# Optimization experiments

Measured on AMD Instinct MI355X. Metric: run time of the kernel, lower is better.

Reference implementation:

```python
import jax, jax.numpy as jnp
import numpy as np

N_NODES = 100000
N_EDGES = 1600000
F_IN = 5
F_HID = 64
F_OUT = 72
NEG_SLOPE = 0.2  # PyG GATConv default


def setup_inputs() -> dict:
    key = jax.random.key(0)
    ks = jax.random.split(key, 8)
    x = jax.random.normal(ks[0], (N_NODES, F_IN), dtype=jnp.float32)
    edge_index = jax.random.randint(ks[1], (2, N_EDGES), 0, N_NODES, dtype=jnp.int64)
    # GATConv params (heads=1, concat=True)
    W = jax.random.normal(ks[2], (F_IN, F_HID), dtype=jnp.float32) * (1.0 / np.sqrt(F_IN))
    att_src = jax.random.normal(ks[3], (F_HID,), dtype=jnp.float32) * (1.0 / np.sqrt(F_HID))
    att_dst = jax.random.normal(ks[4], (F_HID,), dtype=jnp.float32) * (1.0 / np.sqrt(F_HID))
    b_gat = jnp.zeros((F_HID,), dtype=jnp.float32)
    # feature_extractor: Linear(64 -> 72) + ReLU
    W_fc = jax.random.normal(ks[5], (F_HID, F_OUT), dtype=jnp.float32) * (1.0 / np.sqrt(F_HID))
    b_fc = jnp.zeros((F_OUT,), dtype=jnp.float32)
    return {"x": x, "edge_index": edge_index, "W": W, "att_src": att_src,
            "att_dst": att_dst, "b_gat": b_gat, "W_fc": W_fc, "b_fc": b_fc}


def _gat_forward(x, edge_index, W, att_src, att_dst, b_gat, W_fc, b_fc):
    N = x.shape[0]
    h = x @ W  # [N, F_HID]
    # add self loops (PyG GATConv default add_self_loops=True)
    loops = jnp.arange(N, dtype=edge_index.dtype)
    src = jnp.concatenate([edge_index[0], loops])  # [E + N]
    dst = jnp.concatenate([edge_index[1], loops])
    # per-node attention halves, gathered per edge
    a_s = h @ att_src  # [N]
    a_d = h @ att_dst  # [N]
    e = a_s[src] + a_d[dst]  # [E + N]
    e = jnp.where(e > 0, e, NEG_SLOPE * e)  # LeakyReLU
    # edge-softmax grouped by destination node
    m = jax.ops.segment_max(e, dst, num_segments=N)  # self loops => no empty segment
    ex = jnp.exp(e - m[dst])
    denom = jax.ops.segment_sum(ex, dst, num_segments=N)
    alpha = ex / (denom[dst] + 1e-16)
    # weighted scatter-add aggregation
    out = jax.ops.segment_sum(alpha[:, None] * h[src], dst, num_segments=N) + b_gat  # [N, F_HID]
    pooled = jnp.mean(out, axis=0, keepdims=True)  # [1, F_HID]
    return jax.nn.relu(pooled @ W_fc + b_fc)  # [1, F_OUT]


def reference(x, edge_index, W, att_src, att_dst, b_gat, W_fc, b_fc):
    return _gat_forward(x, edge_index, W, att_src, att_dst, b_gat, W_fc, b_fc)
```

## Files before the change

kernel.cpp:

```cpp
#include <hip/hip_runtime.h>


#define NR 25
#define RSHIFT 12
#define RSZ 4096
#define RMASK 4095
#define BBIN 256
#define BINTHR 1024
#define T 8
#define PXE_BLOCKS 512

__global__ __launch_bounds__(256) void k_att(
    const float* __restrict__ x, const float* __restrict__ W,
    const float* __restrict__ att_src, const float* __restrict__ att_dst,
    float* __restrict__ a_s, float* __restrict__ a_d, int N) {
  const int lane = threadIdx.x & 63;
  const int n = blockIdx.x * 4 + (threadIdx.x >> 6);
  if (n >= N) return;
  const float x0 = x[n * 5 + 0], x1 = x[n * 5 + 1], x2 = x[n * 5 + 2],
              x3 = x[n * 5 + 3], x4 = x[n * 5 + 4];
  float hv = x0 * W[0 * 64 + lane];
  hv += x1 * W[1 * 64 + lane];
  hv += x2 * W[2 * 64 + lane];
  hv += x3 * W[3 * 64 + lane];
  hv += x4 * W[4 * 64 + lane];
  float t1 = hv * att_src[lane];
  float t2 = hv * att_dst[lane];
#pragma unroll
  for (int o = 32; o > 0; o >>= 1) {
    t1 += __shfl_xor(t1, o, 64);
    t2 += __shfl_xor(t2, o, 64);
  }
  if (lane == 0) {
    a_s[n] = t1;
    a_d[n] = t2;
  }
}

__global__ __launch_bounds__(BINTHR) void k_cnt(const int* __restrict__ ei,
                                                int* __restrict__ counts,
                                                int E) {
  __shared__ int cd[NR];
  if (threadIdx.x < NR) cd[threadIdx.x] = 0;
  __syncthreads();
  const int chunk = (E + BBIN - 1) / BBIN;
  const int lo = blockIdx.x * chunk;
  const int hi = (lo + chunk < E) ? lo + chunk : E;
#pragma unroll 4
  for (int j = lo + threadIdx.x; j < hi; j += BINTHR)
    atomicAdd(&cd[ei[E + j] >> RSHIFT], 1);
  __syncthreads();
  if (threadIdx.x < NR)
    counts[threadIdx.x * BBIN + blockIdx.x] = cd[threadIdx.x];
}

__global__ __launch_bounds__(BINTHR) void k_scan1(const int* __restrict__ counts,
                                                  int* __restrict__ offs,
                                                  int* __restrict__ rinfo) {
  __shared__ int lc[NR * BBIN];
  __shared__ int tot[NR], base[NR];
  for (int i = threadIdx.x; i < NR * BBIN; i += BINTHR) lc[i] = counts[i];
  __syncthreads();
  if (threadIdx.x < NR) {
    int s = 0;
    const int* row = &lc[threadIdx.x * BBIN];
    for (int b = 0; b < BBIN; ++b) s += row[b];
    tot[threadIdx.x] = s;
  }
  __syncthreads();
  if (threadIdx.x == 0) {
    int a = 0;
    for (int r = 0; r < NR; ++r) {
      base[r] = a;
      a += tot[r];
    }
  }
  __syncthreads();
  if (threadIdx.x < NR) {
    int run = base[threadIdx.x];
    int* orow = &offs[threadIdx.x * BBIN];
    const int* row = &lc[threadIdx.x * BBIN];
    for (int b = 0; b < BBIN; ++b) {
      orow[b] = run;
      run += row[b];
    }
    rinfo[threadIdx.x] = base[threadIdx.x];
    rinfo[NR + threadIdx.x] = tot[threadIdx.x];
  }
}

__global__ __launch_bounds__(BINTHR) void k_scat(
    const int* __restrict__ ei, const float* __restrict__ a_s,
    const float* __restrict__ a_d, const int* __restrict__ offs,
    uint2* __restrict__ rec, int E) {
  __shared__ int cur[NR];
  if (threadIdx.x < NR)
    cur[threadIdx.x] = offs[threadIdx.x * BBIN + blockIdx.x];
  __syncthreads();
  const int chunk = (E + BBIN - 1) / BBIN;
  const int lo = blockIdx.x * chunk;
  const int hi = (lo + chunk < E) ? lo + chunk : E;
#pragma unroll 2
  for (int j = lo + threadIdx.x; j < hi; j += BINTHR) {
    const int s = ei[j];
    const int d = ei[E + j];
    float e = a_s[s] + a_d[d];
    e = e > 0.f ? e : 0.2f * e;
    const float ex = __expf(e);
    const int slot = atomicAdd(&cur[d >> RSHIFT], 1);
    rec[slot] = make_uint2((unsigned)(d & RMASK), __float_as_uint(ex));
  }
}

__global__ __launch_bounds__(256) void k_hist(const uint2* __restrict__ rec,
                                              const int* __restrict__ rinfo,
                                              float* __restrict__ slab) {
  __shared__ float hist[RSZ];
  const int r = blockIdx.x / T;
  const int t = blockIdx.x % T;
  for (int i = threadIdx.x; i < RSZ; i += 256) hist[i] = 0.f;
  __syncthreads();
  const int base = rinfo[r];
  const int tot = rinfo[NR + r];
  const int L = (tot + T - 1) / T;
  const int lo = base + t * L;
  const int hh = (t + 1) * L < tot ? (t + 1) * L : tot;
  const int hi = base + hh;
#pragma unroll 4
  for (int j = lo + threadIdx.x; j < hi; j += 256) {
    const uint2 rv = rec[j];
    atomicAdd(&hist[rv.x], __uint_as_float(rv.y));
  }
  __syncthreads();
  float* outp = slab + ((size_t)(r * T + t)) * RSZ;
  for (int i = threadIdx.x; i < RSZ; i += 256) outp[i] = hist[i];
}

__global__ __launch_bounds__(256) void k_rden(const float* __restrict__ slab,
                                              const float* __restrict__ a_s,
                                              const float* __restrict__ a_d,
                                              float* __restrict__ rden, int N) {
  const int n = blockIdx.x * 256 + threadIdx.x;
  if (n >= N) return;
  const int g = n >> RSHIFT;
  const int i = n & RMASK;
  const float* sp = slab + (size_t)g * T * RSZ + i;
  float sum = 0.f;
#pragma unroll
  for (int t = 0; t < T; ++t) sum += sp[(size_t)t * RSZ];
  float e = a_s[n] + a_d[n];
  e = e > 0.f ? e : 0.2f * e;
  rden[n] = 1.0f / (sum + __expf(e) + 1e-16f);
}

__global__ __launch_bounds__(256) void k_pxe(
    const int* __restrict__ ei, const float* __restrict__ a_s,
    const float* __restrict__ a_d, const float* __restrict__ rden,
    const float* __restrict__ x, float* __restrict__ partial, int E, int N) {
  float a0 = 0.f, a1 = 0.f, a2 = 0.f, a3 = 0.f, a4 = 0.f;
  for (int j = blockIdx.x * 256 + threadIdx.x; j < E; j += gridDim.x * 256) {
    const int s = ei[j];
    const int d = ei[E + j];
    float e = a_s[s] + a_d[d];
    e = e > 0.f ? e : 0.2f * e;
    const float w = __expf(e) * rden[d];
    const float* xp = x + (size_t)s * 5;
    a0 += w * xp[0];
    a1 += w * xp[1];
    a2 += w * xp[2];
    a3 += w * xp[3];
    a4 += w * xp[4];
  }
  for (int n = blockIdx.x * 256 + threadIdx.x; n < N; n += gridDim.x * 256) {
    float e = a_s[n] + a_d[n];
    e = e > 0.f ? e : 0.2f * e;
    const float w = __expf(e) * rden[n];
    const float* xp = x + (size_t)n * 5;
    a0 += w * xp[0];
    a1 += w * xp[1];
    a2 += w * xp[2];
    a3 += w * xp[3];
    a4 += w * xp[4];
  }
#pragma unroll
  for (int o = 32; o > 0; o >>= 1) {
    a0 += __shfl_xor(a0, o, 64);
    a1 += __shfl_xor(a1, o, 64);
    a2 += __shfl_xor(a2, o, 64);
    a3 += __shfl_xor(a3, o, 64);
    a4 += __shfl_xor(a4, o, 64);
  }
  __shared__ float s5[4][5];
  const int lane = threadIdx.x & 63;
  const int w = threadIdx.x >> 6;
  if (lane == 0) {
    s5[w][0] = a0;
    s5[w][1] = a1;
    s5[w][2] = a2;
    s5[w][3] = a3;
    s5[w][4] = a4;
  }
  __syncthreads();
  if (threadIdx.x < 5)
    partial[blockIdx.x * 5 + threadIdx.x] =
        s5[0][threadIdx.x] + s5[1][threadIdx.x] + s5[2][threadIdx.x] +
        s5[3][threadIdx.x];
}

__global__ __launch_bounds__(256) void k_fin(
    const float* __restrict__ partial, const float* __restrict__ W,
    const float* __restrict__ b_gat, const float* __restrict__ W_fc,
    const float* __restrict__ b_fc, float* __restrict__ out, float invN) {
  __shared__ float pp[PXE_BLOCKS * 5];
  __shared__ float px[5];
  __shared__ float pooled[64];
  const int t = threadIdx.x;
  for (int i = t; i < PXE_BLOCKS * 5; i += 256) pp[i] = partial[i];
  __syncthreads();
  if (t < 5) {
    float s = 0.f;
    for (int b = 0; b < PXE_BLOCKS; ++b) s += pp[b * 5 + t];
    px[t] = s * invN;
  }
  __syncthreads();
  if (t < 64) {
    float s = b_gat[t];
#pragma unroll
    for (int k = 0; k < 5; ++k) s += px[k] * W[k * 64 + t];
    pooled[t] = s;
  }
  __syncthreads();
  if (t < 72) {
    float s = b_fc[t];
#pragma unroll
    for (int f = 0; f < 64; ++f) s += pooled[f] * W_fc[f * 72 + t];
    out[t] = s > 0.f ? s : 0.f;
  }
}

extern "C" void kernel_launch(void* const* d_in, const int* in_sizes, int n_in,
                              void* d_out, int out_size, void* d_ws,
                              size_t ws_size, hipStream_t stream) {
  const float* x = (const float*)d_in[0];
  const int* ei = (const int*)d_in[1];
  const float* W = (const float*)d_in[2];
  const float* att_src = (const float*)d_in[3];
  const float* att_dst = (const float*)d_in[4];
  const float* b_gat = (const float*)d_in[5];
  const float* W_fc = (const float*)d_in[6];
  const float* b_fc = (const float*)d_in[7];
  float* out = (float*)d_out;

  const int N = in_sizes[0] / 5;
  const int E = in_sizes[1] / 2;

  char* p = (char*)d_ws;
  auto alloc = [&](size_t nbytes) -> void* {
    void* r = (void*)p;
    p += (nbytes + 255) & ~(size_t)255;
    return r;
  };
  float* a_s = (float*)alloc((size_t)N * sizeof(float));
  float* a_d = (float*)alloc((size_t)N * sizeof(float));
  float* rden = (float*)alloc((size_t)N * sizeof(float));
  int* counts = (int*)alloc((size_t)NR * BBIN * sizeof(int));
  int* offs = (int*)alloc((size_t)NR * BBIN * sizeof(int));
  int* rinfo = (int*)alloc((size_t)2 * NR * sizeof(int));
  uint2* rec = (uint2*)alloc((size_t)E * sizeof(uint2));
  float* slab = (float*)alloc((size_t)NR * T * RSZ * sizeof(float));
  float* partial = (float*)alloc((size_t)PXE_BLOCKS * 5 * sizeof(float));

  k_att<<<(N + 3) / 4, 256, 0, stream>>>(x, W, att_src, att_dst, a_s, a_d, N);
  k_cnt<<<BBIN, BINTHR, 0, stream>>>(ei, counts, E);
  k_scan1<<<1, BINTHR, 0, stream>>>(counts, offs, rinfo);
  k_scat<<<BBIN, BINTHR, 0, stream>>>(ei, a_s, a_d, offs, rec, E);
  k_hist<<<NR * T, 256, 0, stream>>>(rec, rinfo, slab);
  k_rden<<<(N + 255) / 256, 256, 0, stream>>>(slab, a_s, a_d, rden, N);
  k_pxe<<<PXE_BLOCKS, 256, 0, stream>>>(ei, a_s, a_d, rden, x, partial, E, N);
  k_fin<<<1, 256, 0, stream>>>(partial, W, b_gat, W_fc, b_fc, out,
                               1.0f / (float)N);
}
```

Baseline: 168.1 us.

## Reuse binned edge records for weighted aggregation and fuse att/count kernels

The count kernel is merged into the attention-projection kernel by block index, and the denominator kernel is fused with the self-loop aggregation. Binned edge records now carry the source index (uint4), so the final aggregation reads the records grouped by destination range. Per-range reciprocal denominators are cached in LDS instead of being gathered, and exp is not recomputed. In exchange the record buffer doubles in size, which adds write and read traffic in the scatter and histogram passes.

```diff
diff --git a/kernel.cpp b/kernel.cpp
--- a/kernel.cpp
+++ b/kernel.cpp
@@ -6,60 +6,63 @@
 #define RSZ 4096
 #define RMASK 4095
 #define BBIN 256
-#define BINTHR 1024
+#define SCTHR 1024
 #define T 8
-#define PXE_BLOCKS 512
-
-__global__ __launch_bounds__(256) void k_att(
+#define HTHR 512
+#define TP 16
+#define PTHR 512
+#define MAXPART 1024
+
+__global__ __launch_bounds__(256) void k_attcnt(
     const float* __restrict__ x, const float* __restrict__ W,
     const float* __restrict__ att_src, const float* __restrict__ att_dst,
-    float* __restrict__ a_s, float* __restrict__ a_d, int N) {
-  const int lane = threadIdx.x & 63;
-  const int n = blockIdx.x * 4 + (threadIdx.x >> 6);
-  if (n >= N) return;
-  const float x0 = x[n * 5 + 0], x1 = x[n * 5 + 1], x2 = x[n * 5 + 2],
-              x3 = x[n * 5 + 3], x4 = x[n * 5 + 4];
-  float hv = x0 * W[0 * 64 + lane];
-  hv += x1 * W[1 * 64 + lane];
-  hv += x2 * W[2 * 64 + lane];
-  hv += x3 * W[3 * 64 + lane];
-  hv += x4 * W[4 * 64 + lane];
-  float t1 = hv * att_src[lane];
-  float t2 = hv * att_dst[lane];
-#pragma unroll
-  for (int o = 32; o > 0; o >>= 1) {
-    t1 += __shfl_xor(t1, o, 64);
-    t2 += __shfl_xor(t2, o, 64);
-  }
-  if (lane == 0) {
-    a_s[n] = t1;
-    a_d[n] = t2;
-  }
-}
-
-__global__ __launch_bounds__(BINTHR) void k_cnt(const int* __restrict__ ei,
-                                                int* __restrict__ counts,
-                                                int E) {
+    float* __restrict__ a_s, float* __restrict__ a_d,
+    const int* __restrict__ ei, int* __restrict__ counts, int N, int E,
+    int NA) {
   __shared__ int cd[NR];
-  if (threadIdx.x < NR) cd[threadIdx.x] = 0;
-  __syncthreads();
-  const int chunk = (E + BBIN - 1) / BBIN;
-  const int lo = blockIdx.x * chunk;
-  const int hi = (lo + chunk < E) ? lo + chunk : E;
+  if ((int)blockIdx.x < NA) {
+    const int lane = threadIdx.x & 63;
+    const int n = blockIdx.x * 4 + (threadIdx.x >> 6);
+    if (n >= N) return;
+    const float x0 = x[n * 5 + 0], x1 = x[n * 5 + 1], x2 = x[n * 5 + 2],
+                x3 = x[n * 5 + 3], x4 = x[n * 5 + 4];
+    float hv = x0 * W[0 * 64 + lane];
+    hv += x1 * W[1 * 64 + lane];
+    hv += x2 * W[2 * 64 + lane];
+    hv += x3 * W[3 * 64 + lane];
+    hv += x4 * W[4 * 64 + lane];
+    float t1 = hv * att_src[lane];
+    float t2 = hv * att_dst[lane];
+#pragma unroll
+    for (int o = 32; o > 0; o >>= 1) {
+      t1 += __shfl_xor(t1, o, 64);
+      t2 += __shfl_xor(t2, o, 64);
+    }
+    if (lane == 0) {
+      a_s[n] = t1;
+      a_d[n] = t2;
+    }
+  } else {
+    const int b = blockIdx.x - NA;
+    if (threadIdx.x < NR) cd[threadIdx.x] = 0;
+    __syncthreads();
+    const int chunk = (E + BBIN - 1) / BBIN;
+    const int lo = b * chunk;
+    const int hi = (lo + chunk < E) ? lo + chunk : E;
 #pragma unroll 4
-  for (int j = lo + threadIdx.x; j < hi; j += BINTHR)
-    atomicAdd(&cd[ei[E + j] >> RSHIFT], 1);
-  __syncthreads();
-  if (threadIdx.x < NR)
-    counts[threadIdx.x * BBIN + blockIdx.x] = cd[threadIdx.x];
-}
-
-__global__ __launch_bounds__(BINTHR) void k_scan1(const int* __restrict__ counts,
-                                                  int* __restrict__ offs,
-                                                  int* __restrict__ rinfo) {
+    for (int j = lo + threadIdx.x; j < hi; j += 256)
+      atomicAdd(&cd[ei[E + j] >> RSHIFT], 1);
+    __syncthreads();
+    if (threadIdx.x < NR) counts[threadIdx.x * BBIN + b] = cd[threadIdx.x];
+  }
+}
+
+__global__ __launch_bounds__(1024) void k_scan1(const int* __restrict__ counts,
+                                                int* __restrict__ offs,
+                                                int* __restrict__ rinfo) {
   __shared__ int lc[NR * BBIN];
   __shared__ int tot[NR], base[NR];
-  for (int i = threadIdx.x; i < NR * BBIN; i += BINTHR) lc[i] = counts[i];
+  for (int i = threadIdx.x; i < NR * BBIN; i += 1024) lc[i] = counts[i];
   __syncthreads();
   if (threadIdx.x < NR) {
     int s = 0;
@@ -89,10 +92,10 @@
   }
 }
 
-__global__ __launch_bounds__(BINTHR) void k_scat(
+__global__ __launch_bounds__(SCTHR) void k_scat(
     const int* __restrict__ ei, const float* __restrict__ a_s,
     const float* __restrict__ a_d, const int* __restrict__ offs,
-    uint2* __restrict__ rec, int E) {
+    uint4* __restrict__ rec, int E) {
   __shared__ int cur[NR];
   if (threadIdx.x < NR)
     cur[threadIdx.x] = offs[threadIdx.x * BBIN + blockIdx.x];
@@ -101,24 +104,25 @@
   const int lo = blockIdx.x * chunk;
   const int hi = (lo + chunk < E) ? lo + chunk : E;
 #pragma unroll 2
-  for (int j = lo + threadIdx.x; j < hi; j += BINTHR) {
+  for (int j = lo + threadIdx.x; j < hi; j += SCTHR) {
     const int s = ei[j];
     const int d = ei[E + j];
     float e = a_s[s] + a_d[d];
     e = e > 0.f ? e : 0.2f * e;
     const float ex = __expf(e);
     const int slot = atomicAdd(&cur[d >> RSHIFT], 1);
-    rec[slot] = make_uint2((unsigned)(d & RMASK), __float_as_uint(ex));
-  }
-}
-
-__global__ __launch_bounds__(256) void k_hist(const uint2* __restrict__ rec,
-                                              const int* __restrict__ rinfo,
-                                              float* __restrict__ slab) {
+    rec[slot] = make_uint4((unsigned)(d & RMASK), __float_as_uint(ex),
+                           (unsigned)s, 0u);
+  }
+}
+
+__global__ __launch_bounds__(HTHR) void k_hist(const uint4* __restrict__ rec,
+                                               const int* __restrict__ rinfo,
+                                               float* __restrict__ slab) {
   __shared__ float hist[RSZ];
   const int r = blockIdx.x / T;
   const int t = blockIdx.x % T;
-  for (int i = threadIdx.x; i < RSZ; i += 256) hist[i] = 0.f;
+  for (int i = threadIdx.x; i < RSZ; i += HTHR) hist[i] = 0.f;
   __syncthreads();
   const int base = rinfo[r];
   const int tot = rinfo[NR + r];
@@ -127,60 +131,40 @@
   const int hh = (t + 1) * L < tot ? (t + 1) * L : tot;
   const int hi = base + hh;
 #pragma unroll 4
-  for (int j = lo + threadIdx.x; j < hi; j += 256) {
-    const uint2 rv = rec[j];
+  for (int j = lo + threadIdx.x; j < hi; j += HTHR) {
+    const uint4 rv = rec[j];
     atomicAdd(&hist[rv.x], __uint_as_float(rv.y));
   }
   __syncthreads();
   float* outp = slab + ((size_t)(r * T + t)) * RSZ;
-  for (int i = threadIdx.x; i < RSZ; i += 256) outp[i] = hist[i];
-}
-
-__global__ __launch_bounds__(256) void k_rden(const float* __restrict__ slab,
-                                              const float* __restrict__ a_s,
-                                              const float* __restrict__ a_d,
-                                              float* __restrict__ rden, int N) {
+  for (int i = threadIdx.x; i < RSZ; i += HTHR) outp[i] = hist[i];
+}
+
+__global__ __launch_bounds__(256) void k_rdenpx(
+    const float* __restrict__ slab, const float* __restrict__ a_s,
+    const float* __restrict__ a_d, const float* __restrict__ x,
+    float* __restrict__ rden, float* __restrict__ partial, int N, int pbase) {
   const int n = blockIdx.x * 256 + threadIdx.x;
-  if (n >= N) return;
-  const int g = n >> RSHIFT;
-  const int i = n & RMASK;
-  const float* sp = slab + (size_t)g * T * RSZ + i;
-  float sum = 0.f;
-#pragma unroll
-  for (int t = 0; t < T; ++t) sum += sp[(size_t)t * RSZ];
-  float e = a_s[n] + a_d[n];
-  e = e > 0.f ? e : 0.2f * e;
-  rden[n] = 1.0f / (sum + __expf(e) + 1e-16f);
-}
-
-__global__ __launch_bounds__(256) void k_pxe(
-    const int* __restrict__ ei, const float* __restrict__ a_s,
-    const float* __restrict__ a_d, const float* __restrict__ rden,
-    const float* __restrict__ x, float* __restrict__ partial, int E, int N) {
   float a0 = 0.f, a1 = 0.f, a2 = 0.f, a3 = 0.f, a4 = 0.f;
-  for (int j = blockIdx.x * 256 + threadIdx.x; j < E; j += gridDim.x * 256) {
-    const int s = ei[j];
-    const int d = ei[E + j];
-    float e = a_s[s] + a_d[d];
-    e = e > 0.f ? e : 0.2f * e;
-    const float w = __expf(e) * rden[d];
-    const float* xp = x + (size_t)s * 5;
-    a0 += w * xp[0];
-    a1 += w * xp[1];
-    a2 += w * xp[2];
-    a3 += w * xp[3];
-    a4 += w * xp[4];
-  }
-  for (int n = blockIdx.x * 256 + threadIdx.x; n < N; n += gridDim.x * 256) {
+  if (n < N) {
+    const int g = n >> RSHIFT;
+    const int i = n & RMASK;
+    const float* sp = slab + (size_t)g * T * RSZ + i;
+    float sum = 0.f;
+#pragma unroll
+    for (int t = 0; t < T; ++t) sum += sp[(size_t)t * RSZ];
     float e = a_s[n] + a_d[n];
     e = e > 0.f ? e : 0.2f * e;
-    const float w = __expf(e) * rden[n];
+    const float exs = __expf(e);
+    const float r = 1.0f / (sum + exs + 1e-16f);
+    rden[n] = r;
+    const float w = exs * r;
     const float* xp = x + (size_t)n * 5;
-    a0 += w * xp[0];
-    a1 += w * xp[1];
-    a2 += w * xp[2];
-    a3 += w * xp[3];
-    a4 += w * xp[4];
+    a0 = w * xp[0];
+    a1 = w * xp[1];
+    a2 = w * xp[2];
+    a3 = w * xp[3];
+    a4 = w * xp[4];
   }
 #pragma unroll
   for (int o = 32; o > 0; o >>= 1) {
@@ -202,24 +186,84 @@
   }
   __syncthreads();
   if (threadIdx.x < 5)
-    partial[blockIdx.x * 5 + threadIdx.x] =
+    partial[(size_t)(pbase + blockIdx.x) * 5 + threadIdx.x] =
         s5[0][threadIdx.x] + s5[1][threadIdx.x] + s5[2][threadIdx.x] +
         s5[3][threadIdx.x];
 }
 
+__global__ __launch_bounds__(PTHR) void k_pxr(const uint4* __restrict__ rec,
+                                              const int* __restrict__ rinfo,
+                                              const float* __restrict__ rden,
+                                              const float* __restrict__ x,
+                                              float* __restrict__ partial,
+                                              int N) {
+  __shared__ float rlds[RSZ];
+  const int r = blockIdx.x / TP;
+  const int t = blockIdx.x % TP;
+  const int gbase = r * RSZ;
+  for (int i = threadIdx.x; i < RSZ; i += PTHR) {
+    const int gi = gbase + i;
+    rlds[i] = (gi < N) ? rden[gi] : 0.f;
+  }
+  __syncthreads();
+  const int base = rinfo[r];
+  const int tot = rinfo[NR + r];
+  const int L = (tot + TP - 1) / TP;
+  const int lo = base + t * L;
+  const int hh = (t + 1) * L < tot ? (t + 1) * L : tot;
+  const int hi = base + hh;
+  float a0 = 0.f, a1 = 0.f, a2 = 0.f, a3 = 0.f, a4 = 0.f;
+#pragma unroll 2
+  for (int j = lo + threadIdx.x; j < hi; j += PTHR) {
+    const uint4 rv = rec[j];
+    const float w = __uint_as_float(rv.y) * rlds[rv.x];
+    const float* xp = x + (size_t)rv.z * 5;
+    a0 += w * xp[0];
+    a1 += w * xp[1];
+    a2 += w * xp[2];
+    a3 += w * xp[3];
+    a4 += w * xp[4];
+  }
+#pragma unroll
+  for (int o = 32; o > 0; o >>= 1) {
+    a0 += __shfl_xor(a0, o, 64);
+    a1 += __shfl_xor(a1, o, 64);
+    a2 += __shfl_xor(a2, o, 64);
+    a3 += __shfl_xor(a3, o, 64);
+    a4 += __shfl_xor(a4, o, 64);
+  }
+  __shared__ float s5[PTHR / 64][5];
+  const int lane = threadIdx.x & 63;
+  const int w = threadIdx.x >> 6;
+  if (lane == 0) {
+    s5[w][0] = a0;
+    s5[w][1] = a1;
+    s5[w][2] = a2;
+    s5[w][3] = a3;
+    s5[w][4] = a4;
+  }
+  __syncthreads();
+  if (threadIdx.x < 5) {
+    float s = 0.f;
+#pragma unroll
+    for (int ww = 0; ww < PTHR / 64; ++ww) s += s5[ww][threadIdx.x];
+    partial[(size_t)blockIdx.x * 5 + threadIdx.x] = s;
+  }
+}
+
 __global__ __launch_bounds__(256) void k_fin(
-    const float* __restrict__ partial, const float* __restrict__ W,
+    const float* __restrict__ partial, int nparts, const float* __restrict__ W,
     const float* __restrict__ b_gat, const float* __restrict__ W_fc,
     const float* __restrict__ b_fc, float* __restrict__ out, float invN) {
-  __shared__ float pp[PXE_BLOCKS * 5];
+  __shared__ float pp[MAXPART * 5];
   __shared__ float px[5];
   __shared__ float pooled[64];
   const int t = threadIdx.x;
-  for (int i = t; i < PXE_BLOCKS * 5; i += 256) pp[i] = partial[i];
+  for (int i = t; i < nparts * 5; i += 256) pp[i] = partial[i];
   __syncthreads();
   if (t < 5) {
     float s = 0.f;
-    for (int b = 0; b < PXE_BLOCKS; ++b) s += pp[b * 5 + t];
+    for (int b = 0; b < nparts; ++b) s += pp[b * 5 + t];
     px[t] = s * invN;
   }
   __syncthreads();
@@ -253,6 +297,9 @@
 
   const int N = in_sizes[0] / 5;
   const int E = in_sizes[1] / 2;
+  const int NA = (N + 3) / 4;
+  const int RDB = (N + 255) / 256;
+  const int nparts = NR * TP + RDB;
 
   char* p = (char*)d_ws;
   auto alloc = [&](size_t nbytes) -> void* {
@@ -266,17 +313,18 @@
   int* counts = (int*)alloc((size_t)NR * BBIN * sizeof(int));
   int* offs = (int*)alloc((size_t)NR * BBIN * sizeof(int));
   int* rinfo = (int*)alloc((size_t)2 * NR * sizeof(int));
-  uint2* rec = (uint2*)alloc((size_t)E * sizeof(uint2));
+  uint4* rec = (uint4*)alloc((size_t)E * sizeof(uint4));
   float* slab = (float*)alloc((size_t)NR * T * RSZ * sizeof(float));
-  float* partial = (float*)alloc((size_t)PXE_BLOCKS * 5 * sizeof(float));
-
-  k_att<<<(N + 3) / 4, 256, 0, stream>>>(x, W, att_src, att_dst, a_s, a_d, N);
-  k_cnt<<<BBIN, BINTHR, 0, stream>>>(ei, counts, E);
-  k_scan1<<<1, BINTHR, 0, stream>>>(counts, offs, rinfo);
-  k_scat<<<BBIN, BINTHR, 0, stream>>>(ei, a_s, a_d, offs, rec, E);
-  k_hist<<<NR * T, 256, 0, stream>>>(rec, rinfo, slab);
-  k_rden<<<(N + 255) / 256, 256, 0, stream>>>(slab, a_s, a_d, rden, N);
-  k_pxe<<<PXE_BLOCKS, 256, 0, stream>>>(ei, a_s, a_d, rden, x, partial, E, N);
-  k_fin<<<1, 256, 0, stream>>>(partial, W, b_gat, W_fc, b_fc, out,
+  float* partial = (float*)alloc((size_t)MAXPART * 5 * sizeof(float));
+
+  k_attcnt<<<NA + BBIN, 256, 0, stream>>>(x, W, att_src, att_dst, a_s, a_d, ei,
+                                          counts, N, E, NA);
+  k_scan1<<<1, 1024, 0, stream>>>(counts, offs, rinfo);
+  k_scat<<<BBIN, SCTHR, 0, stream>>>(ei, a_s, a_d, offs, rec, E);
+  k_hist<<<NR * T, HTHR, 0, stream>>>(rec, rinfo, slab);
+  k_rdenpx<<<RDB, 256, 0, stream>>>(slab, a_s, a_d, x, rden, partial, N,
+                                    NR * TP);
+  k_pxr<<<NR * TP, PTHR, 0, stream>>>(rec, rinfo, rden, x, partial, N);
+  k_fin<<<1, 256, 0, stream>>>(partial, nparts, W, b_gat, W_fc, b_fc, out,
                                1.0f / (float)N);
 }
```

New measurement: 166.0 us. About the same (-1.3%).
